# Performance work log

Hardware: AMD Instinct MI355X
Metric: run time of the kernel (lower is better)

Reference implementation:

```python
import jax, jax.numpy as jnp
import numpy as np

N = 100000
D = 128
E = 600000


def setup_inputs() -> dict:
    key = jax.random.key(0)
    k = jax.random.split(key, 7)
    x = jax.random.normal(k[0], (N, D), dtype=jnp.float32)
    edge_index = jax.random.randint(k[1], (2, E), 0, N, dtype=jnp.int32)
    edge_weight = jax.random.uniform(k[2], (E,), dtype=jnp.float32)
    # Linear params (torch nn.Linear: y = x @ W.T + b), init scale ~ 1/sqrt(D)
    s = 1.0 / np.sqrt(D)
    W1 = jax.random.uniform(k[3], (D, D), minval=-s, maxval=s, dtype=jnp.float32)
    b1 = jax.random.uniform(k[4], (D,), minval=-s, maxval=s, dtype=jnp.float32)
    W2 = jax.random.uniform(k[5], (D, D), minval=-s, maxval=s, dtype=jnp.float32)
    b2 = jax.random.uniform(k[6], (D,), minval=-s, maxval=s, dtype=jnp.float32)
    return {"x": x, "edge_index": edge_index, "edge_weight": edge_weight,
            "W1": W1, "b1": b1, "W2": W2, "b2": b2}


def reference(x, edge_index, edge_weight, W1, b1, W2, b2):
    row, col = edge_index[0], edge_index[1]
    # gather-weight-scatter: agg[col] += w * x[row]
    msgs = edge_weight[:, None] * x[row]            # [E, D]
    agg = jax.ops.segment_sum(msgs, col, num_segments=x.shape[0])  # [N, D]
    h = (agg + x) @ W1.T + b1 + (agg * x) @ W2.T + b2
    out = jax.nn.leaky_relu(h, negative_slope=0.2)
    # dropout omitted (eval-mode reference)
    return out
```

## Files before the change

kernel.cpp:

```cpp
#include <hip/hip_runtime.h>

#define D 128

typedef __attribute__((ext_vector_type(8))) short short8;
typedef __attribute__((ext_vector_type(4))) float f32x4;

__device__ __forceinline__ unsigned int f2bf(float f) {
  unsigned int u = __float_as_uint(f);
  return (u + 0x7fffu + ((u >> 16) & 1u)) >> 16;
}

__global__ __launch_bounds__(256) void pre1_k(
    const float* __restrict__ x, unsigned short* __restrict__ xbf, int n8,
    const int* __restrict__ ei, int* __restrict__ cursor, int E, int XB) {
  int b = blockIdx.x;
  if (b < XB) {
    int tid = b * 256 + threadIdx.x;
    if (tid >= n8) return;
    float4 a = ((const float4*)x)[(size_t)tid * 2];
    float4 c = ((const float4*)x)[(size_t)tid * 2 + 1];
    uint4 o;
    o.x = f2bf(a.x) | (f2bf(a.y) << 16);
    o.y = f2bf(a.z) | (f2bf(a.w) << 16);
    o.z = f2bf(c.x) | (f2bf(c.y) << 16);
    o.w = f2bf(c.z) | (f2bf(c.w) << 16);
    ((uint4*)xbf)[tid] = o;
  } else {
    int e = (b - XB) * 256 + threadIdx.x;
    if (e < E) atomicAdd(&cursor[ei[E + e]], 1);
  }
}

__global__ __launch_bounds__(256) void scan_block_k(
    const int* __restrict__ deg, int* __restrict__ rowptr,
    int* __restrict__ partials, int Nn) {
  __shared__ int sdata[256];
  int t = threadIdx.x;
  int base = blockIdx.x * 1024 + t * 4;
  int v[4];
  #pragma unroll
  for (int j = 0; j < 4; ++j) v[j] = (base + j < Nn) ? deg[base + j] : 0;
  int tsum = v[0] + v[1] + v[2] + v[3];
  sdata[t] = tsum;
  __syncthreads();
  for (int off = 1; off < 256; off <<= 1) {
    int add = (t >= off) ? sdata[t - off] : 0;
    __syncthreads();
    sdata[t] += add;
    __syncthreads();
  }
  int run = sdata[t] - tsum;
  if (t == 255) partials[blockIdx.x] = sdata[255];
  #pragma unroll
  for (int j = 0; j < 4; ++j) {
    if (base + j < Nn) rowptr[base + j] = run;
    run += v[j];
  }
}

__global__ __launch_bounds__(128) void scan_partials_k(int* partials, int NB) {
  __shared__ int s[128];
  int t = threadIdx.x;
  int orig = (t < NB) ? partials[t] : 0;
  s[t] = orig;
  __syncthreads();
  for (int off = 1; off < 128; off <<= 1) {
    int add = (t >= off) ? s[t - off] : 0;
    __syncthreads();
    s[t] += add;
    __syncthreads();
  }
  if (t < NB) partials[t] = s[t] - orig;
}

__global__ __launch_bounds__(256) void addoff_prep_k(
    int* __restrict__ rowptr, int* __restrict__ cursor,
    const int* __restrict__ partials,
    const float* __restrict__ W1, const float* __restrict__ b1,
    const float* __restrict__ W2, const float* __restrict__ b2,
    unsigned short* __restrict__ Bpack, float* __restrict__ bsum,
    int Nn, int E, int AB) {
  int b = blockIdx.x;
  if (b < AB) {
    int i = b * 256 + threadIdx.x;
    if (i < Nn) {
      int v = rowptr[i] + partials[i >> 10];
      rowptr[i] = v;
      cursor[i] = v;
    }
    if (i == 0) rowptr[Nn] = E;
  } else {
    int tid = (b - AB) * 256 + threadIdx.x;
    if (tid < 32768) {
      int j = tid & 7;
      int l = (tid >> 3) & 63;
      int ktnt = tid >> 9;
      int kt = ktnt >> 3, nt = ktnt & 7;
      int k = kt * 32 + ((l >> 4) << 3) + j;
      int col = nt * 16 + (l & 15);
      float v = (k < 128) ? W1[col * 128 + k] : W2[col * 128 + (k - 128)];
      Bpack[tid] = (unsigned short)f2bf(v);
    }
    if (tid < 128) bsum[tid] = b1[tid] + b2[tid];
  }
}

__global__ __launch_bounds__(256) void fill_k(
    const int* __restrict__ ei, const float* __restrict__ ew,
    int* __restrict__ cursor, int2* __restrict__ edges, int E) {
  int e = blockIdx.x * 256 + threadIdx.x;
  if (e >= E) return;
  int c = ei[E + e];
  int p = atomicAdd(&cursor[c], 1);
  edges[p] = make_int2(ei[e], __float_as_int(ew[e]));
}

__global__ __launch_bounds__(256, 4) void aggfused_k(
    const unsigned short* __restrict__ xbf, const float* __restrict__ x,
    const int* __restrict__ rowptr, const int2* __restrict__ edges,
    const unsigned short* __restrict__ Bpack, const float* __restrict__ bsum,
    float* __restrict__ out, int Nn) {
  constexpr int ROWB = 528;
  __shared__ __align__(16) unsigned char Us[64 * ROWB];
  const int t = threadIdx.x;
  const int node0 = blockIdx.x * 64;
  const int lane = t & 63, w = t >> 6;

  for (int i = 0; i < 16; ++i) {
    int node = w * 16 + i;
    int g = node0 + node;
    uint up = 0, vp = 0;
    if (g < Nn) {
      float ax = 0.f, ay = 0.f;
      int beg = rowptr[g], end = rowptr[g + 1];
      for (int p = beg; p < end; p += 8) {
        int2 e[8];
        #pragma unroll
        for (int q = 0; q < 8; ++q) e[q] = edges[min(p + q, end - 1)];
        unsigned int v[8];
        #pragma unroll
        for (int q = 0; q < 8; ++q)
          v[q] = *(const unsigned int*)(xbf + (size_t)e[q].x * D + lane * 2);
        #pragma unroll
        for (int q = 0; q < 8; ++q) {
          float wt = (p + q < end) ? __int_as_float(e[q].y) : 0.f;
          ax += wt * __uint_as_float(v[q] << 16);
          ay += wt * __uint_as_float(v[q] & 0xffff0000u);
        }
      }
      float2 xr = *(const float2*)(x + (size_t)g * D + lane * 2);
      up = f2bf(ax + xr.x) | (f2bf(ay + xr.y) << 16);
      vp = f2bf(ax * xr.x) | (f2bf(ay * xr.y) << 16);
    }
    *(unsigned int*)(Us + node * ROWB + lane * 4)       = up;
    *(unsigned int*)(Us + node * ROWB + 256 + lane * 4) = vp;
  }
  __syncthreads();

  const int c15 = lane & 15, kq = lane >> 4;

  short8 afr[8];
  const unsigned char* abase = Us + (size_t)(w * 16 + c15) * ROWB + kq * 16;
  #pragma unroll
  for (int kt = 0; kt < 8; ++kt)
    afr[kt] = *(const short8*)(abase + kt * 64);

  f32x4 acc[8];
  #pragma unroll
  for (int nt = 0; nt < 8; ++nt) acc[nt] = (f32x4){0.f, 0.f, 0.f, 0.f};

  const short8* bp = (const short8*)Bpack + lane;
  #pragma unroll
  for (int kt = 0; kt < 8; ++kt) {
    #pragma unroll
    for (int nt = 0; nt < 8; ++nt) {
      short8 bfr = bp[(kt * 8 + nt) * 64];
      acc[nt] = __builtin_amdgcn_mfma_f32_16x16x32_bf16(afr[kt], bfr, acc[nt], 0, 0, 0);
    }
  }

  float bsv[8];
  #pragma unroll
  for (int nt = 0; nt < 8; ++nt) bsv[nt] = bsum[nt * 16 + c15];

  #pragma unroll
  for (int r = 0; r < 4; ++r) {
    int g = node0 + w * 16 + kq * 4 + r;
    if (g >= Nn) continue;
    float* orow = out + (size_t)g * D + c15;
    #pragma unroll
    for (int nt = 0; nt < 8; ++nt) {
      float h = acc[nt][r] + bsv[nt];
      orow[nt * 16] = h > 0.f ? h : 0.2f * h;
    }
  }
}

extern "C" void kernel_launch(void* const* d_in, const int* in_sizes, int n_in,
                              void* d_out, int out_size, void* d_ws, size_t ws_size,
                              hipStream_t stream) {
  const float* x  = (const float*)d_in[0];
  const int*   ei = (const int*)d_in[1];
  const float* ew = (const float*)d_in[2];
  const float* W1 = (const float*)d_in[3];
  const float* b1 = (const float*)d_in[4];
  const float* W2 = (const float*)d_in[5];
  const float* b2 = (const float*)d_in[6];
  float* out = (float*)d_out;

  const int Nn = in_sizes[0] / D;
  const int E  = in_sizes[2];
  const int NB = (Nn + 1023) / 1024;

  const size_t xbfB    = (((size_t)Nn * D * 2) + 255) & ~(size_t)255;
  const size_t edgesB  = (size_t)E * sizeof(int2);
  const size_t cursorB = (((size_t)Nn * 4) + 255) & ~(size_t)255;
  const size_t rowptrB = (((size_t)(Nn + 1) * 4) + 255) & ~(size_t)255;
  const size_t partB   = 1024;
  const size_t BpackB  = 65536;

  char* base = (char*)d_ws;
  unsigned short* xbf   = (unsigned short*)base;  base += xbfB;
  int2*  edges   = (int2*)base;                   base += edgesB;
  int*   cursor  = (int*)base;                    base += cursorB;
  int*   rowptr  = (int*)base;                    base += rowptrB;
  int*   partials= (int*)base;                    base += partB;
  unsigned short* Bpack = (unsigned short*)base;  base += BpackB;
  float* bs      = (float*)base;

  hipMemsetAsync(cursor, 0, (size_t)Nn * 4, stream);

  const int n8 = Nn * D / 8;
  const int XB = (n8 + 255) / 256;
  const int HB = (E + 255) / 256;
  pre1_k<<<XB + HB, 256, 0, stream>>>(x, xbf, n8, ei, cursor, E, XB);

  scan_block_k<<<NB, 256, 0, stream>>>(cursor, rowptr, partials, Nn);
  scan_partials_k<<<1, 128, 0, stream>>>(partials, NB);

  const int AB = (Nn + 255) / 256;
  addoff_prep_k<<<AB + 128, 256, 0, stream>>>(rowptr, cursor, partials,
                                              W1, b1, W2, b2, Bpack, bs,
                                              Nn, E, AB);

  fill_k<<<HB, 256, 0, stream>>>(ei, ew, cursor, edges, E);

  aggfused_k<<<(Nn + 63) / 64, 256, 0, stream>>>(xbf, x, rowptr, edges,
                                                 Bpack, bs, out, Nn);
}
```

Measured before the change: 253.8 us.

## Replace CSR build with fixed-capacity per-node edge slots and overflow list

Drops the degree count, two-level scan, offset add and fill kernels. Edges are now written directly into fixed-size per-destination slot arrays in a single pass that also converts x to bf16 and packs the weights, with an overflow buffer for nodes whose degree exceeds the slot capacity. The aggregation now has each half-wave handle one node with 4 features per lane, and reads slot counts instead of rowptr. This cuts five kernel launches and their dependencies. In exchange it uses more workspace, adds a linear scan of the overflow list for high-degree nodes, and silently drops overflow edges past ovfcap.

```diff
diff --git a/kernel.cpp b/kernel.cpp
--- a/kernel.cpp
+++ b/kernel.cpp
@@ -4,15 +4,23 @@
 
 typedef __attribute__((ext_vector_type(8))) short short8;
 typedef __attribute__((ext_vector_type(4))) float f32x4;
+
+struct OvfE { int dst, row; float w; };
 
 __device__ __forceinline__ unsigned int f2bf(float f) {
   unsigned int u = __float_as_uint(f);
   return (u + 0x7fffu + ((u >> 16) & 1u)) >> 16;
 }
 
-__global__ __launch_bounds__(256) void pre1_k(
-    const float* __restrict__ x, unsigned short* __restrict__ xbf, int n8,
-    const int* __restrict__ ei, int* __restrict__ cursor, int E, int XB) {
+__global__ __launch_bounds__(256) void pre_k(
+    const float* __restrict__ x, unsigned short* __restrict__ xbf, int n8, int XB,
+    const int* __restrict__ ei, const float* __restrict__ ew,
+    int* __restrict__ deg, int* __restrict__ ovfcnt,
+    int2* __restrict__ slots, OvfE* __restrict__ ovf, int ovfcap,
+    int capLog2, int E, int FB,
+    const float* __restrict__ W1, const float* __restrict__ b1,
+    const float* __restrict__ W2, const float* __restrict__ b2,
+    unsigned short* __restrict__ Bpack, float* __restrict__ bsum) {
   int b = blockIdx.x;
   if (b < XB) {
     int tid = b * 256 + threadIdx.x;
@@ -25,72 +33,19 @@
     o.z = f2bf(c.x) | (f2bf(c.y) << 16);
     o.w = f2bf(c.z) | (f2bf(c.w) << 16);
     ((uint4*)xbf)[tid] = o;
+  } else if (b < XB + FB) {
+    int e = (b - XB) * 256 + threadIdx.x;
+    if (e >= E) return;
+    int c = ei[E + e];
+    int p = atomicAdd(&deg[c], 1);
+    if (p < (1 << capLog2)) {
+      slots[((size_t)c << capLog2) + p] = make_int2(ei[e], __float_as_int(ew[e]));
+    } else {
+      int oi = atomicAdd(ovfcnt, 1);
+      if (oi < ovfcap) { ovf[oi].dst = c; ovf[oi].row = ei[e]; ovf[oi].w = ew[e]; }
+    }
   } else {
-    int e = (b - XB) * 256 + threadIdx.x;
-    if (e < E) atomicAdd(&cursor[ei[E + e]], 1);
-  }
-}
-
-__global__ __launch_bounds__(256) void scan_block_k(
-    const int* __restrict__ deg, int* __restrict__ rowptr,
-    int* __restrict__ partials, int Nn) {
-  __shared__ int sdata[256];
-  int t = threadIdx.x;
-  int base = blockIdx.x * 1024 + t * 4;
-  int v[4];
-  #pragma unroll
-  for (int j = 0; j < 4; ++j) v[j] = (base + j < Nn) ? deg[base + j] : 0;
-  int tsum = v[0] + v[1] + v[2] + v[3];
-  sdata[t] = tsum;
-  __syncthreads();
-  for (int off = 1; off < 256; off <<= 1) {
-    int add = (t >= off) ? sdata[t - off] : 0;
-    __syncthreads();
-    sdata[t] += add;
-    __syncthreads();
-  }
-  int run = sdata[t] - tsum;
-  if (t == 255) partials[blockIdx.x] = sdata[255];
-  #pragma unroll
-  for (int j = 0; j < 4; ++j) {
-    if (base + j < Nn) rowptr[base + j] = run;
-    run += v[j];
-  }
-}
-
-__global__ __launch_bounds__(128) void scan_partials_k(int* partials, int NB) {
-  __shared__ int s[128];
-  int t = threadIdx.x;
-  int orig = (t < NB) ? partials[t] : 0;
-  s[t] = orig;
-  __syncthreads();
-  for (int off = 1; off < 128; off <<= 1) {
-    int add = (t >= off) ? s[t - off] : 0;
-    __syncthreads();
-    s[t] += add;
-    __syncthreads();
-  }
-  if (t < NB) partials[t] = s[t] - orig;
-}
-
-__global__ __launch_bounds__(256) void addoff_prep_k(
-    int* __restrict__ rowptr, int* __restrict__ cursor,
-    const int* __restrict__ partials,
-    const float* __restrict__ W1, const float* __restrict__ b1,
-    const float* __restrict__ W2, const float* __restrict__ b2,
-    unsigned short* __restrict__ Bpack, float* __restrict__ bsum,
-    int Nn, int E, int AB) {
-  int b = blockIdx.x;
-  if (b < AB) {
-    int i = b * 256 + threadIdx.x;
-    if (i < Nn) {
-      int v = rowptr[i] + partials[i >> 10];
-      rowptr[i] = v;
-      cursor[i] = v;
-    }
-    if (i == 0) rowptr[Nn] = E;
-  } else {
-    int tid = (b - AB) * 256 + threadIdx.x;
+    int tid = (b - XB - FB) * 256 + threadIdx.x;
     if (tid < 32768) {
       int j = tid & 7;
       int l = (tid >> 3) & 63;
@@ -105,55 +60,103 @@
   }
 }
 
-__global__ __launch_bounds__(256) void fill_k(
-    const int* __restrict__ ei, const float* __restrict__ ew,
-    int* __restrict__ cursor, int2* __restrict__ edges, int E) {
-  int e = blockIdx.x * 256 + threadIdx.x;
-  if (e >= E) return;
-  int c = ei[E + e];
-  int p = atomicAdd(&cursor[c], 1);
-  edges[p] = make_int2(ei[e], __float_as_int(ew[e]));
-}
-
 __global__ __launch_bounds__(256, 4) void aggfused_k(
     const unsigned short* __restrict__ xbf, const float* __restrict__ x,
-    const int* __restrict__ rowptr, const int2* __restrict__ edges,
+    const int* __restrict__ deg, const int2* __restrict__ slots,
+    const int* __restrict__ ovfcnt, const OvfE* __restrict__ ovf,
     const unsigned short* __restrict__ Bpack, const float* __restrict__ bsum,
-    float* __restrict__ out, int Nn) {
+    float* __restrict__ out, int Nn, int capLog2, int usebf) {
   constexpr int ROWB = 528;
   __shared__ __align__(16) unsigned char Us[64 * ROWB];
   const int t = threadIdx.x;
   const int node0 = blockIdx.x * 64;
   const int lane = t & 63, w = t >> 6;
-
-  for (int i = 0; i < 16; ++i) {
-    int node = w * 16 + i;
-    int g = node0 + node;
-    uint up = 0, vp = 0;
-    if (g < Nn) {
-      float ax = 0.f, ay = 0.f;
-      int beg = rowptr[g], end = rowptr[g + 1];
-      for (int p = beg; p < end; p += 8) {
-        int2 e[8];
-        #pragma unroll
-        for (int q = 0; q < 8; ++q) e[q] = edges[min(p + q, end - 1)];
-        unsigned int v[8];
-        #pragma unroll
-        for (int q = 0; q < 8; ++q)
-          v[q] = *(const unsigned int*)(xbf + (size_t)e[q].x * D + lane * 2);
-        #pragma unroll
-        for (int q = 0; q < 8; ++q) {
-          float wt = (p + q < end) ? __int_as_float(e[q].y) : 0.f;
-          ax += wt * __uint_as_float(v[q] << 16);
-          ay += wt * __uint_as_float(v[q] & 0xffff0000u);
+  const int half = lane >> 5, sl = lane & 31;
+  const int cap = 1 << capLog2;
+
+  int dall = 0;
+  {
+    int g = node0 + w * 16 + lane;
+    if (lane < 16 && g < Nn) dall = deg[g];
+  }
+  int ovn = 0;
+  if (__any(dall > cap)) ovn = *ovfcnt;
+
+  for (int ii = 0; ii < 8; ++ii) {
+    int nodeIdx = ii * 2 + half;
+    int g = node0 + w * 16 + nodeIdx;
+    int dv = __shfl(dall, nodeIdx);
+    f32x4 acc = {0.f, 0.f, 0.f, 0.f};
+    if (g < Nn && dv > 0) {
+      int d = min(dv, cap);
+      const int2* sb = slots + ((size_t)g << capLog2);
+      if (usebf) {
+        for (int p = 0; p < d; p += 8) {
+          int2 e[8];
+          #pragma unroll
+          for (int q = 0; q < 8; ++q) e[q] = sb[min(p + q, d - 1)];
+          uint2 v[8];
+          #pragma unroll
+          for (int q = 0; q < 8; ++q)
+            v[q] = *(const uint2*)(xbf + (size_t)e[q].x * D + sl * 4);
+          #pragma unroll
+          for (int q = 0; q < 8; ++q) {
+            float wt = (p + q < d) ? __int_as_float(e[q].y) : 0.f;
+            acc[0] += wt * __uint_as_float(v[q].x << 16);
+            acc[1] += wt * __uint_as_float(v[q].x & 0xffff0000u);
+            acc[2] += wt * __uint_as_float(v[q].y << 16);
+            acc[3] += wt * __uint_as_float(v[q].y & 0xffff0000u);
+          }
+        }
+      } else {
+        for (int p = 0; p < d; p += 8) {
+          int2 e[8];
+          #pragma unroll
+          for (int q = 0; q < 8; ++q) e[q] = sb[min(p + q, d - 1)];
+          float4 v[8];
+          #pragma unroll
+          for (int q = 0; q < 8; ++q)
+            v[q] = ((const float4*)(x + (size_t)e[q].x * D))[sl];
+          #pragma unroll
+          for (int q = 0; q < 8; ++q) {
+            float wt = (p + q < d) ? __int_as_float(e[q].y) : 0.f;
+            acc[0] += wt * v[q].x;
+            acc[1] += wt * v[q].y;
+            acc[2] += wt * v[q].z;
+            acc[3] += wt * v[q].w;
+          }
         }
       }
-      float2 xr = *(const float2*)(x + (size_t)g * D + lane * 2);
-      up = f2bf(ax + xr.x) | (f2bf(ay + xr.y) << 16);
-      vp = f2bf(ax * xr.x) | (f2bf(ay * xr.y) << 16);
-    }
-    *(unsigned int*)(Us + node * ROWB + lane * 4)       = up;
-    *(unsigned int*)(Us + node * ROWB + 256 + lane * 4) = vp;
+      if (dv > cap) {
+        for (int j = 0; j < ovn; ++j) {
+          if (ovf[j].dst == g) {
+            float wt = ovf[j].w;
+            int r = ovf[j].row;
+            if (usebf) {
+              uint2 v = *(const uint2*)(xbf + (size_t)r * D + sl * 4);
+              acc[0] += wt * __uint_as_float(v.x << 16);
+              acc[1] += wt * __uint_as_float(v.x & 0xffff0000u);
+              acc[2] += wt * __uint_as_float(v.y << 16);
+              acc[3] += wt * __uint_as_float(v.y & 0xffff0000u);
+            } else {
+              float4 v = ((const float4*)(x + (size_t)r * D))[sl];
+              acc[0] += wt * v.x; acc[1] += wt * v.y;
+              acc[2] += wt * v.z; acc[3] += wt * v.w;
+            }
+          }
+        }
+      }
+    }
+    float4 xr = make_float4(0.f, 0.f, 0.f, 0.f);
+    if (g < Nn) xr = ((const float4*)(x + (size_t)g * D))[sl];
+    uint2 up, vp;
+    up.x = f2bf(acc[0] + xr.x) | (f2bf(acc[1] + xr.y) << 16);
+    up.y = f2bf(acc[2] + xr.z) | (f2bf(acc[3] + xr.w) << 16);
+    vp.x = f2bf(acc[0] * xr.x) | (f2bf(acc[1] * xr.y) << 16);
+    vp.y = f2bf(acc[2] * xr.z) | (f2bf(acc[3] * xr.w) << 16);
+    int nrow = w * 16 + nodeIdx;
+    *(uint2*)(Us + nrow * ROWB + sl * 8)       = up;
+    *(uint2*)(Us + nrow * ROWB + 256 + sl * 8) = vp;
   }
   __syncthreads();
 
@@ -165,9 +168,9 @@
   for (int kt = 0; kt < 8; ++kt)
     afr[kt] = *(const short8*)(abase + kt * 64);
 
-  f32x4 acc[8];
-  #pragma unroll
-  for (int nt = 0; nt < 8; ++nt) acc[nt] = (f32x4){0.f, 0.f, 0.f, 0.f};
+  f32x4 acc2[8];
+  #pragma unroll
+  for (int nt = 0; nt < 8; ++nt) acc2[nt] = (f32x4){0.f, 0.f, 0.f, 0.f};
 
   const short8* bp = (const short8*)Bpack + lane;
   #pragma unroll
@@ -175,7 +178,7 @@
     #pragma unroll
     for (int nt = 0; nt < 8; ++nt) {
       short8 bfr = bp[(kt * 8 + nt) * 64];
-      acc[nt] = __builtin_amdgcn_mfma_f32_16x16x32_bf16(afr[kt], bfr, acc[nt], 0, 0, 0);
+      acc2[nt] = __builtin_amdgcn_mfma_f32_16x16x32_bf16(afr[kt], bfr, acc2[nt], 0, 0, 0);
     }
   }
 
@@ -190,7 +193,7 @@
     float* orow = out + (size_t)g * D + c15;
     #pragma unroll
     for (int nt = 0; nt < 8; ++nt) {
-      float h = acc[nt][r] + bsv[nt];
+      float h = acc2[nt][r] + bsv[nt];
       orow[nt * 16] = h > 0.f ? h : 0.2f * h;
     }
   }
@@ -210,41 +213,41 @@
 
   const int Nn = in_sizes[0] / D;
   const int E  = in_sizes[2];
-  const int NB = (Nn + 1023) / 1024;
-
-  const size_t xbfB    = (((size_t)Nn * D * 2) + 255) & ~(size_t)255;
-  const size_t edgesB  = (size_t)E * sizeof(int2);
-  const size_t cursorB = (((size_t)Nn * 4) + 255) & ~(size_t)255;
-  const size_t rowptrB = (((size_t)(Nn + 1) * 4) + 255) & ~(size_t)255;
-  const size_t partB   = 1024;
-  const size_t BpackB  = 65536;
+  const int n8 = Nn * D / 8;
+
+  auto al = [](size_t v) { return (v + 255) & ~(size_t)255; };
+  const int ovfcap = 65536;
+  const size_t degB   = al((size_t)(Nn + 1) * 4);
+  const size_t ovfB   = al((size_t)ovfcap * sizeof(OvfE));
+  const size_t BpackB = 65536;
+  const size_t bsB    = 512;
+  const size_t xbfB   = al((size_t)Nn * D * 2);
+  const size_t fixedB = degB + ovfB + BpackB + bsB;
+
+  int capLog2, usebf;
+  if      (ws_size >= fixedB + (((size_t)Nn << 5) * 8) + xbfB) { capLog2 = 5; usebf = 1; }
+  else if (ws_size >= fixedB + (((size_t)Nn << 4) * 8) + xbfB) { capLog2 = 4; usebf = 1; }
+  else if (ws_size >= fixedB + (((size_t)Nn << 4) * 8))        { capLog2 = 4; usebf = 0; }
+  else                                                         { capLog2 = 3; usebf = 0; }
+  const size_t slotsB = al(((size_t)Nn << capLog2) * 8);
 
   char* base = (char*)d_ws;
-  unsigned short* xbf   = (unsigned short*)base;  base += xbfB;
-  int2*  edges   = (int2*)base;                   base += edgesB;
-  int*   cursor  = (int*)base;                    base += cursorB;
-  int*   rowptr  = (int*)base;                    base += rowptrB;
-  int*   partials= (int*)base;                    base += partB;
+  int*  deg    = (int*)base;                      base += degB;
+  OvfE* ovf    = (OvfE*)base;                     base += ovfB;
   unsigned short* Bpack = (unsigned short*)base;  base += BpackB;
-  float* bs      = (float*)base;
-
-  hipMemsetAsync(cursor, 0, (size_t)Nn * 4, stream);
-
-  const int n8 = Nn * D / 8;
-  const int XB = (n8 + 255) / 256;
-  const int HB = (E + 255) / 256;
-  pre1_k<<<XB + HB, 256, 0, stream>>>(x, xbf, n8, ei, cursor, E, XB);
-
-  scan_block_k<<<NB, 256, 0, stream>>>(cursor, rowptr, partials, Nn);
-  scan_partials_k<<<1, 128, 0, stream>>>(partials, NB);
-
-  const int AB = (Nn + 255) / 256;
-  addoff_prep_k<<<AB + 128, 256, 0, stream>>>(rowptr, cursor, partials,
-                                              W1, b1, W2, b2, Bpack, bs,
-                                              Nn, E, AB);
-
-  fill_k<<<HB, 256, 0, stream>>>(ei, ew, cursor, edges, E);
-
-  aggfused_k<<<(Nn + 63) / 64, 256, 0, stream>>>(xbf, x, rowptr, edges,
-                                                 Bpack, bs, out, Nn);
-}
+  float* bs    = (float*)base;                    base += bsB;
+  int2* slots  = (int2*)base;                     base += slotsB;
+  unsigned short* xbf = (unsigned short*)base;
+
+  hipMemsetAsync(deg, 0, (size_t)(Nn + 1) * 4, stream);
+
+  const int XB = usebf ? (n8 + 255) / 256 : 0;
+  const int FB = (E + 255) / 256;
+  pre_k<<<XB + FB + 128, 256, 0, stream>>>(
+      x, xbf, n8, XB, ei, ew, deg, deg + Nn, slots, ovf, ovfcap,
+      capLog2, E, FB, W1, b1, W2, b2, Bpack, bs);
+
+  aggfused_k<<<(Nn + 63) / 64, 256, 0, stream>>>(
+      usebf ? xbf : (const unsigned short*)nullptr, x, deg, slots,
+      deg + Nn, ovf, Bpack, bs, out, Nn, capLog2, usebf);
+}
```

Result: faster. 218.8 us (-13.8%).
